# Performance work log

Hardware: AMD Instinct MI355X
Metric: run time of the kernel (lower is better)

The kernel has to match this reference:

```python
import jax, jax.numpy as jnp
import numpy as np
import math

NLAT, NLON, LMAX, MMAX = 128, 256, 50, 50
K = 3  # three_nn

# ---- precompute: Clenshaw-Curtis quadrature (torch_harmonics 'equiangular') ----
def _cc_nodes_weights(n):
    Nn = n - 1
    theta = np.pi * np.arange(n) / Nn
    v = np.zeros(n)
    for k in range(1, Nn // 2 + 1):
        b = 1.0 if 2 * k == Nn else 2.0
        v += b * np.cos(2 * k * theta) / (4 * k * k - 1)
    w = (2.0 / Nn) * (1.0 - v)
    w[0] *= 0.5
    w[-1] *= 0.5
    return np.cos(theta), w

# ---- precompute: orthonormal associated Legendre P_l^m(cos theta), csphase ----
def _legpoly(lmax, mmax, cost):
    sint = np.sqrt(np.clip(1.0 - cost ** 2, 0.0, None))
    p = np.zeros((mmax, lmax, cost.shape[0]))
    pmm = np.full(cost.shape[0], np.sqrt(1.0 / (4.0 * np.pi)))
    for m in range(mmax):
        if m > 0:
            pmm = -pmm * np.sqrt((2.0 * m + 1.0) / (2.0 * m)) * sint
        p[m, m] = pmm
        if m + 1 < lmax:
            p[m, m + 1] = np.sqrt(2.0 * m + 3.0) * cost * pmm
        for l in range(m + 2, lmax):
            a = np.sqrt((4.0 * l * l - 1.0) / (l * l - m * m))
            b = np.sqrt(((2.0 * l + 1.0) * (l - 1 + m) * (l - 1 - m)) / ((2.0 * l - 3.0) * (l * l - m * m)))
            p[m, l] = a * cost * p[m, l - 1] - b * p[m, l - 2]
    return p

_cost, _w = _cc_nodes_weights(NLAT)
_PCTW = jnp.asarray((_legpoly(LMAX, MMAX, _cost) * _w[None, None, :]).astype(np.float32))  # (mmax,lmax,nlat)

_gx, _gy = np.meshgrid(np.arange(NLAT), np.arange(-NLAT, NLAT), indexing='ij')
_GRID = jnp.asarray((np.stack([_gx.ravel(), _gy.ravel()], -1) / NLAT * np.pi).astype(np.float32))  # (M,2)

_RECTW = jnp.asarray(np.exp(-(LMAX - np.arange(1, LMAX + 1)) ** 2 / (2.0 * LMAX ** 2)).astype(np.float32))  # (lmax,)


def to_spherical(coords):
    # coords: (B,N,3) -> r:(B,N), sph:(B,N,2) = [arccos(x/r), azimuth in [0,2pi)]
    sq = coords ** 2
    pn = jnp.sqrt(jnp.flip(jnp.cumsum(jnp.flip(sq, -1), -1), -1))  # pn[...,i] = ||coords[...,i:]||
    r = pn[..., 0]
    phi = jnp.arccos(coords[..., :-2] / pn[..., :-2])
    a = jnp.arccos(coords[..., -2] / pn[..., -2])
    phi_final = a + (2.0 * math.pi - 2.0 * a) * (coords[..., -1] < 0)
    return r, jnp.concatenate([phi, phi_final[..., None]], axis=-1)


def interp_to_grid(coords):
    # spherical transform + 3-NN (squared dists) + distance-weighted interpolation onto the lat/lon grid
    r, sph = to_spherical(coords)
    sph = sph.at[..., 1].add(-math.pi)
    # brute-force pairwise squared distances grid(M,2) vs sph(B,N,2): (B,M,N)
    d2 = (jnp.sum(_GRID ** 2, -1)[None, :, None] + jnp.sum(sph ** 2, -1)[:, None, :]
          - 2.0 * jnp.einsum('md,bnd->bmn', _GRID, sph))
    _, idx = jax.lax.top_k(-jax.lax.stop_gradient(d2), K)  # (B,M,K), ascending distance
    sel = jax.vmap(lambda s, i: s[i])(sph, idx)            # (B,M,K,2)
    fsel = jax.vmap(lambda f, i: f[i])(r, idx)             # (B,M,K)
    dk = jnp.sum((_GRID[None, :, None, :] - sel) ** 2, -1)  # recompute selected sq-dists (differentiable)
    w = dk / jnp.sum(dk, -1, keepdims=True)                # weights = dist / sum(dist), as in source
    return jnp.sum(fsel * w, -1).reshape(-1, NLAT, NLON)


def sht_real(x):
    # RealSHT (equiangular, ortho): rfft(norm='forward')*2pi, then Legendre*quadrature einsum; real part only
    xf = jnp.fft.rfft(x, axis=-1)[..., :MMAX] * (2.0 * math.pi / NLON)
    return jnp.einsum('bkm,mlk->blm', jnp.real(xf).astype(jnp.float32), _PCTW)  # (B,lmax,mmax)


def setup_inputs() -> dict:
    key = jax.random.key(0)
    k1, k2 = jax.random.split(key)
    pred = jax.random.normal(k1, (2, 2048, 3), dtype=jnp.float32)
    target = jax.random.normal(k2, (2, 2048, 3), dtype=jnp.float32)
    return {"pred": pred, "target": target}


def reference(pred, target):
    pc = sht_real(interp_to_grid(pred))
    tc = sht_real(interp_to_grid(target))
    return jnp.mean(jnp.sum((pc - tc) ** 2 * _RECTW[None, :, None], axis=(1, 2)))
```

## Files before the change

### kernel.cpp

```cpp
#include <hip/hip_runtime.h>
#include <math.h>

#define PI_D 3.14159265358979323846
#define PIF  3.14159265358979323846f
#define NLAT 128
#define NLON 256
#define LMAX 50
#define MMAX 50
#define NPTS 2048
#define NBT 16
#define NBA 32
#define NBIN (NBT * NBA)
#define WBIN 0.19634954084936207f
#define INVW 5.092958178940651f
#define BIG 1e30f
#define KMASK 0xFFFFF800u

__device__ __forceinline__ void insert3(float kf, float& k0, float& k1, float& k2) {
    float n1 = __builtin_amdgcn_fmed3f(kf, k0, k1);
    float n2 = __builtin_amdgcn_fmed3f(kf, k1, k2);
    k0 = fminf(kf, k0);
    k1 = n1;
    k2 = n2;
}

__device__ __forceinline__ float mkkey(float gt, float gl, float2 tl, int idx) {
    float dt = gt - tl.x, dl = gl - tl.y;
    float d = fmaf(dt, dt, dl * dl);
    return __uint_as_float((__float_as_uint(d) & KMASK) | (unsigned)idx);
}

__global__ __launch_bounds__(256) void fused_main(
    const float* __restrict__ pred, const float* __restrict__ tgt,
    float* __restrict__ pctwT, float* __restrict__ fre, float* __restrict__ out) {

    __shared__ float2 s_btl[NPTS];
    __shared__ float  s_br[NPTS];
    __shared__ int    s_cnt[NBIN];
    __shared__ int    s_off[NBIN + 1];
    __shared__ float  ctab[NLON];
    __shared__ float  row[NLON];
    __shared__ float  part[256];

    int bid = blockIdx.x;
    int t = threadIdx.x;

    if (bid >= 512) {
        int k = bid - 512;
        int m = t;
        if (k == 0 && m == 0) out[0] = 0.0f;
        if (m >= MMAX) return;

        double thd = PI_D * (double)k / 127.0;
        float cost = (float)cos(thd);
        float sint = (float)sin(thd);

        float c2 = (float)cos(2.0 * thd);
        float two_c2 = 2.0f * c2;
        float cp = 1.0f, cc = c2, v = 0.0f;
        for (int tt = 1; tt <= 63; ++tt) {
            v += 2.0f * cc / (float)(4 * tt * tt - 1);
            float cn = two_c2 * cc - cp;
            cp = cc;
            cc = cn;
        }
        float w = (2.0f / 127.0f) * (1.0f - v);
        if (k == 0 || k == 127) w *= 0.5f;

        float pmm = sqrtf(1.0f / (4.0f * PIF));
        for (int i = 1; i <= m; ++i)
            pmm = -pmm * sqrtf((2.0f * (float)i + 1.0f) / (2.0f * (float)i)) * sint;

        float* o = pctwT + (size_t)k * MMAX + m;
        for (int l = 0; l < m; ++l) o[(size_t)l * NLAT * MMAX] = 0.0f;
        o[(size_t)m * NLAT * MMAX] = pmm * w;
        float plm2 = pmm, plm1 = 0.0f;
        if (m + 1 < LMAX) {
            plm1 = sqrtf(2.0f * (float)m + 3.0f) * cost * pmm;
            o[(size_t)(m + 1) * NLAT * MMAX] = plm1 * w;
        }
        for (int l = m + 2; l < LMAX; ++l) {
            float fl = (float)l;
            float denom = fl * fl - (float)(m * m);
            float a = sqrtf((4.0f * fl * fl - 1.0f) / denom);
            float b = sqrtf(((2.0f * fl + 1.0f) * (float)(l - 1 + m) * (float)(l - 1 - m)) /
                            ((2.0f * fl - 3.0f) * denom));
            float p = a * cost * plm1 - b * plm2;
            o[(size_t)l * NLAT * MMAX] = p * w;
            plm2 = plm1;
            plm1 = p;
        }
        return;
    }

    int f = bid >> 7;
    int lat = bid & 127;
    const float* src = ((f < 2) ? pred : tgt) + (size_t)(f & 1) * NPTS * 3;

    s_cnt[t] = 0;
    s_cnt[t + 256] = 0;
    ctab[t] = (float)cos(2.0 * PI_D * (double)t / (double)NLON);
    __syncthreads();

    float pth[8], paz[8], pr[8];
    int pbin[8];
#pragma unroll
    for (int i = 0; i < 8; ++i) {
        int n = t + 256 * i;
        float x = src[3 * n], y = src[3 * n + 1], z = src[3 * n + 2];
        float s1 = z * z;
        float s2 = s1 + y * y;
        float s3 = s2 + x * x;
        float r = sqrtf(s3);
        float rho = sqrtf(s2);
        float th = acosf(x / r);
        float a = acosf(y / rho);
        float az = (z < 0.0f) ? (a + (2.0f * PIF - 2.0f * a)) : a;
        az -= PIF;
        int bt = min(max((int)(th * INVW), 0), NBT - 1);
        int ba = min(max((int)((az + PIF) * INVW), 0), NBA - 1);
        int b = bt * NBA + ba;
        pth[i] = th; paz[i] = az; pr[i] = r; pbin[i] = b;
        atomicAdd(&s_cnt[b], 1);
    }
    __syncthreads();

    if (t == 0) s_off[NBIN] = NPTS;
    if (t < 64) {
        int base = t * 8;
        int loc[8];
        int run = 0;
#pragma unroll
        for (int i = 0; i < 8; ++i) { loc[i] = run; run += s_cnt[base + i]; }
        int x = run;
#pragma unroll
        for (int d = 1; d < 64; d <<= 1) {
            int y = __shfl_up(x, d);
            if (t >= d) x += y;
        }
        int ex = x - run;
#pragma unroll
        for (int i = 0; i < 8; ++i) s_off[base + i] = ex + loc[i];
    }
    __syncthreads();
    s_cnt[t] = s_off[t];
    s_cnt[t + 256] = s_off[t + 256];
    __syncthreads();
#pragma unroll
    for (int i = 0; i < 8; ++i) {
        int pos = atomicAdd(&s_cnt[pbin[i]], 1);
        s_btl[pos] = make_float2(pth[i], paz[i]);
        s_br[pos] = pr[i];
    }
    __syncthreads();

    int j = t;
    float gt = (float)((double)lat * PI_D / 128.0);
    float gl = (float)(((double)j - 128.0) * PI_D / 128.0);
    float glp = gl + PIF;
    int bt0 = lat >> 3;
    int ba0 = j >> 3;

    auto scan_seg = [&](int i, int i1, float& q0, float& q1, float& q2) {
        for (; i + 4 <= i1; i += 4) {
            float2 a0 = s_btl[i];
            float2 a1 = s_btl[i + 1];
            float2 a2 = s_btl[i + 2];
            float2 a3 = s_btl[i + 3];
            insert3(mkkey(gt, gl, a0, i), q0, q1, q2);
            insert3(mkkey(gt, gl, a1, i + 1), q0, q1, q2);
            insert3(mkkey(gt, gl, a2, i + 2), q0, q1, q2);
            insert3(mkkey(gt, gl, a3, i + 3), q0, q1, q2);
        }
        for (; i < i1; ++i)
            insert3(mkkey(gt, gl, s_btl[i], i), q0, q1, q2);
    };

    float k0 = BIG, k1 = BIG, k2 = BIG;
    {
        int rtl = max(bt0 - 1, 0), rth = min(bt0 + 1, NBT - 1);
        int bal = max(ba0 - 1, 0), bah = min(ba0 + 1, NBA - 1);
        for (int bt = rtl; bt <= rth; ++bt)
            scan_seg(s_off[bt * NBA + bal], s_off[bt * NBA + bah + 1], k0, k1, k2);
    }

    bool done;
    {
        float safe = BIG;
        if (bt0 - 1 > 0)       safe = fminf(safe, gt - (float)(bt0 - 1) * WBIN);
        if (bt0 + 1 < NBT - 1) safe = fminf(safe, (float)(bt0 + 2) * WBIN - gt);
        if (ba0 - 1 > 0)       safe = fminf(safe, glp - (float)(ba0 - 1) * WBIN);
        if (ba0 + 1 < NBA - 1) safe = fminf(safe, (float)(ba0 + 2) * WBIN - glp);
        done = (k2 <= safe * safe);
    }

    for (int R = 2; R <= 31; ++R) {
        if (__all(done)) break;
        if (!done) {
            int btl = bt0 - R, bth = bt0 + R;
            int lo = max(btl, 0), hi = min(bth, NBT - 1);
            int bal = max(ba0 - R, 0), bah = min(ba0 + R, NBA - 1);
            for (int bt = lo; bt <= hi; ++bt) {
                if (bt == btl || bt == bth) {
                    scan_seg(s_off[bt * NBA + bal], s_off[bt * NBA + bah + 1], k0, k1, k2);
                } else {
                    if (ba0 - R >= 0) {
                        int b = bt * NBA + ba0 - R;
                        scan_seg(s_off[b], s_off[b + 1], k0, k1, k2);
                    }
                    if (ba0 + R <= NBA - 1) {
                        int b = bt * NBA + ba0 + R;
                        scan_seg(s_off[b], s_off[b + 1], k0, k1, k2);
                    }
                }
            }
            float safe = BIG;
            if (bt0 - R > 0)       safe = fminf(safe, gt - (float)(bt0 - R) * WBIN);
            if (bt0 + R < NBT - 1) safe = fminf(safe, (float)(bt0 + R + 1) * WBIN - gt);
            if (ba0 - R > 0)       safe = fminf(safe, glp - (float)(ba0 - R) * WBIN);
            if (ba0 + R < NBA - 1) safe = fminf(safe, (float)(ba0 + R + 1) * WBIN - glp);
            if (k2 <= safe * safe) done = true;
        }
    }

    {
        int i0 = __float_as_uint(k0) & 0x7FF;
        int i1 = __float_as_uint(k1) & 0x7FF;
        int i2 = __float_as_uint(k2) & 0x7FF;
        float2 p0 = s_btl[i0];
        float2 p1 = s_btl[i1];
        float2 p2 = s_btl[i2];
        float dt0 = gt - p0.x, dl0 = gl - p0.y;
        float dt1 = gt - p1.x, dl1 = gl - p1.y;
        float dt2 = gt - p2.x, dl2 = gl - p2.y;
        float d0 = fmaf(dt0, dt0, dl0 * dl0);
        float d1 = fmaf(dt1, dt1, dl1 * dl1);
        float d2 = fmaf(dt2, dt2, dl2 * dl2);
        float s = d0 + d1 + d2;
        row[j] = (d0 * s_br[i0] + d1 * s_br[i1] + d2 * s_br[i2]) / s;
    }
    __syncthreads();

    {
        int q = t >> 6;
        int mm = t & 63;
        if (mm < MMAX) {
            int bs = q * 64;
            float a0 = 0.0f, a1 = 0.0f, a2 = 0.0f, a3 = 0.0f;
            int p = (bs * mm) & (NLON - 1);
            int st1 = mm;
            int st2 = (2 * mm) & (NLON - 1);
            int st3 = (3 * mm) & (NLON - 1);
            int st4 = (4 * mm) & (NLON - 1);
            for (int i = 0; i < 64; i += 4) {
                a0 += row[bs + i] * ctab[p];
                a1 += row[bs + i + 1] * ctab[(p + st1) & (NLON - 1)];
                a2 += row[bs + i + 2] * ctab[(p + st2) & (NLON - 1)];
                a3 += row[bs + i + 3] * ctab[(p + st3) & (NLON - 1)];
                p = (p + st4) & (NLON - 1);
            }
            part[q * 64 + mm] = (a0 + a1) + (a2 + a3);
        }
    }
    __syncthreads();
    if (t < MMAX) {
        float v = ((part[t] + part[64 + t]) + (part[128 + t] + part[192 + t])) *
                  (float)(2.0 * PI_D / (double)NLON);
        fre[(f * NLAT + lat) * MMAX + t] = v;
    }
}

__global__ __launch_bounds__(256) void contract_loss(const float* __restrict__ fre,
                                                     const float* __restrict__ pctwT,
                                                     float* __restrict__ out) {
    int b = blockIdx.x / LMAX;
    int l = blockIdx.x % LMAX;
    int mm = threadIdx.x & 63;
    int kq = threadIdx.x >> 6;
    __shared__ float sp[4][64], st_[4][64];
    float pc = 0.0f, tc = 0.0f;
    if (mm < MMAX) {
        const float* pw = pctwT + ((size_t)l * NLAT + kq * 32) * MMAX + mm;
        const float* fp = fre + ((size_t)b * NLAT + kq * 32) * MMAX + mm;
        const float* ft = fre + ((size_t)(2 + b) * NLAT + kq * 32) * MMAX + mm;
#pragma unroll 8
        for (int k = 0; k < 32; ++k) {
            float w = pw[k * MMAX];
            pc += fp[k * MMAX] * w;
            tc += ft[k * MMAX] * w;
        }
    }
    sp[kq][mm] = pc;
    st_[kq][mm] = tc;
    __syncthreads();
    if (threadIdx.x < 64) {
        int m2 = threadIdx.x;
        float pcs = (sp[0][m2] + sp[1][m2]) + (sp[2][m2] + sp[3][m2]);
        float tcs = (st_[0][m2] + st_[1][m2]) + (st_[2][m2] + st_[3][m2]);
        float diff = pcs - tcs;
        double dl_ = (double)(49 - l);
        float rw = (float)exp(-(dl_ * dl_) / 5000.0);
        float contrib = (m2 < MMAX) ? diff * diff * rw * 0.5f : 0.0f;
        for (int off = 32; off > 0; off >>= 1) contrib += __shfl_down(contrib, off);
        if (m2 == 0) atomicAdd(out, contrib);
    }
}

extern "C" void kernel_launch(void* const* d_in, const int* in_sizes, int n_in,
                              void* d_out, int out_size, void* d_ws, size_t ws_size,
                              hipStream_t stream) {
    const float* pred = (const float*)d_in[0];
    const float* tgt = (const float*)d_in[1];
    float* ws = (float*)d_ws;

    float* pctwT = ws;
    float* fre   = ws + 320000;
    float* out = (float*)d_out;

    fused_main<<<640, 256, 0, stream>>>(pred, tgt, pctwT, fre, out);
    contract_loss<<<2 * LMAX, 256, 0, stream>>>(fre, pctwT, out);
}
```

Measured before the change: 84.11 us.

## Merge main and contraction kernels into one cooperative launch with grid sync

Replaces the two-kernel sequence with a single cooperative kernel that runs the grid/Legendre stage, performs a grid-wide sync, then has the first 100 blocks do the Legendre contraction and loss reduction, reusing shared memory. This removes one kernel launch and the inter-kernel gap. In exchange it adds cooperative launch overhead and a grid barrier, and requires all 640 blocks to be co-resident. The cos table also switches from double cos to the fast __cosf intrinsic, trading accuracy for speed.

```diff
diff --git a/kernel.cpp b/kernel.cpp
--- a/kernel.cpp
+++ b/kernel.cpp
@@ -1,5 +1,8 @@
 #include <hip/hip_runtime.h>
+#include <hip/hip_cooperative_groups.h>
 #include <math.h>
+
+namespace cg = cooperative_groups;
 
 #define PI_D 3.14159265358979323846
 #define PIF  3.14159265358979323846f
@@ -30,7 +33,7 @@
     return __uint_as_float((__float_as_uint(d) & KMASK) | (unsigned)idx);
 }
 
-__global__ __launch_bounds__(256) void fused_main(
+__global__ __launch_bounds__(256) void mega_kernel(
     const float* __restrict__ pred, const float* __restrict__ tgt,
     float* __restrict__ pctwT, float* __restrict__ fre, float* __restrict__ out) {
 
@@ -42,6 +45,7 @@
     __shared__ float  row[NLON];
     __shared__ float  part[256];
 
+    cg::grid_group grid = cg::this_grid();
     int bid = blockIdx.x;
     int t = threadIdx.x;
 
@@ -49,260 +53,261 @@
         int k = bid - 512;
         int m = t;
         if (k == 0 && m == 0) out[0] = 0.0f;
-        if (m >= MMAX) return;
-
-        double thd = PI_D * (double)k / 127.0;
-        float cost = (float)cos(thd);
-        float sint = (float)sin(thd);
-
-        float c2 = (float)cos(2.0 * thd);
-        float two_c2 = 2.0f * c2;
-        float cp = 1.0f, cc = c2, v = 0.0f;
-        for (int tt = 1; tt <= 63; ++tt) {
-            v += 2.0f * cc / (float)(4 * tt * tt - 1);
-            float cn = two_c2 * cc - cp;
-            cp = cc;
-            cc = cn;
-        }
-        float w = (2.0f / 127.0f) * (1.0f - v);
-        if (k == 0 || k == 127) w *= 0.5f;
-
-        float pmm = sqrtf(1.0f / (4.0f * PIF));
-        for (int i = 1; i <= m; ++i)
-            pmm = -pmm * sqrtf((2.0f * (float)i + 1.0f) / (2.0f * (float)i)) * sint;
-
-        float* o = pctwT + (size_t)k * MMAX + m;
-        for (int l = 0; l < m; ++l) o[(size_t)l * NLAT * MMAX] = 0.0f;
-        o[(size_t)m * NLAT * MMAX] = pmm * w;
-        float plm2 = pmm, plm1 = 0.0f;
-        if (m + 1 < LMAX) {
-            plm1 = sqrtf(2.0f * (float)m + 3.0f) * cost * pmm;
-            o[(size_t)(m + 1) * NLAT * MMAX] = plm1 * w;
-        }
-        for (int l = m + 2; l < LMAX; ++l) {
-            float fl = (float)l;
-            float denom = fl * fl - (float)(m * m);
-            float a = sqrtf((4.0f * fl * fl - 1.0f) / denom);
-            float b = sqrtf(((2.0f * fl + 1.0f) * (float)(l - 1 + m) * (float)(l - 1 - m)) /
-                            ((2.0f * fl - 3.0f) * denom));
-            float p = a * cost * plm1 - b * plm2;
-            o[(size_t)l * NLAT * MMAX] = p * w;
-            plm2 = plm1;
-            plm1 = p;
-        }
-        return;
-    }
-
-    int f = bid >> 7;
-    int lat = bid & 127;
-    const float* src = ((f < 2) ? pred : tgt) + (size_t)(f & 1) * NPTS * 3;
-
-    s_cnt[t] = 0;
-    s_cnt[t + 256] = 0;
-    ctab[t] = (float)cos(2.0 * PI_D * (double)t / (double)NLON);
-    __syncthreads();
-
-    float pth[8], paz[8], pr[8];
-    int pbin[8];
-#pragma unroll
-    for (int i = 0; i < 8; ++i) {
-        int n = t + 256 * i;
-        float x = src[3 * n], y = src[3 * n + 1], z = src[3 * n + 2];
-        float s1 = z * z;
-        float s2 = s1 + y * y;
-        float s3 = s2 + x * x;
-        float r = sqrtf(s3);
-        float rho = sqrtf(s2);
-        float th = acosf(x / r);
-        float a = acosf(y / rho);
-        float az = (z < 0.0f) ? (a + (2.0f * PIF - 2.0f * a)) : a;
-        az -= PIF;
-        int bt = min(max((int)(th * INVW), 0), NBT - 1);
-        int ba = min(max((int)((az + PIF) * INVW), 0), NBA - 1);
-        int b = bt * NBA + ba;
-        pth[i] = th; paz[i] = az; pr[i] = r; pbin[i] = b;
-        atomicAdd(&s_cnt[b], 1);
-    }
-    __syncthreads();
-
-    if (t == 0) s_off[NBIN] = NPTS;
-    if (t < 64) {
-        int base = t * 8;
-        int loc[8];
-        int run = 0;
-#pragma unroll
-        for (int i = 0; i < 8; ++i) { loc[i] = run; run += s_cnt[base + i]; }
-        int x = run;
-#pragma unroll
-        for (int d = 1; d < 64; d <<= 1) {
-            int y = __shfl_up(x, d);
-            if (t >= d) x += y;
-        }
-        int ex = x - run;
-#pragma unroll
-        for (int i = 0; i < 8; ++i) s_off[base + i] = ex + loc[i];
-    }
-    __syncthreads();
-    s_cnt[t] = s_off[t];
-    s_cnt[t + 256] = s_off[t + 256];
-    __syncthreads();
-#pragma unroll
-    for (int i = 0; i < 8; ++i) {
-        int pos = atomicAdd(&s_cnt[pbin[i]], 1);
-        s_btl[pos] = make_float2(pth[i], paz[i]);
-        s_br[pos] = pr[i];
-    }
-    __syncthreads();
-
-    int j = t;
-    float gt = (float)((double)lat * PI_D / 128.0);
-    float gl = (float)(((double)j - 128.0) * PI_D / 128.0);
-    float glp = gl + PIF;
-    int bt0 = lat >> 3;
-    int ba0 = j >> 3;
-
-    auto scan_seg = [&](int i, int i1, float& q0, float& q1, float& q2) {
-        for (; i + 4 <= i1; i += 4) {
-            float2 a0 = s_btl[i];
-            float2 a1 = s_btl[i + 1];
-            float2 a2 = s_btl[i + 2];
-            float2 a3 = s_btl[i + 3];
-            insert3(mkkey(gt, gl, a0, i), q0, q1, q2);
-            insert3(mkkey(gt, gl, a1, i + 1), q0, q1, q2);
-            insert3(mkkey(gt, gl, a2, i + 2), q0, q1, q2);
-            insert3(mkkey(gt, gl, a3, i + 3), q0, q1, q2);
-        }
-        for (; i < i1; ++i)
-            insert3(mkkey(gt, gl, s_btl[i], i), q0, q1, q2);
-    };
-
-    float k0 = BIG, k1 = BIG, k2 = BIG;
-    {
-        int rtl = max(bt0 - 1, 0), rth = min(bt0 + 1, NBT - 1);
-        int bal = max(ba0 - 1, 0), bah = min(ba0 + 1, NBA - 1);
-        for (int bt = rtl; bt <= rth; ++bt)
-            scan_seg(s_off[bt * NBA + bal], s_off[bt * NBA + bah + 1], k0, k1, k2);
-    }
-
-    bool done;
-    {
-        float safe = BIG;
-        if (bt0 - 1 > 0)       safe = fminf(safe, gt - (float)(bt0 - 1) * WBIN);
-        if (bt0 + 1 < NBT - 1) safe = fminf(safe, (float)(bt0 + 2) * WBIN - gt);
-        if (ba0 - 1 > 0)       safe = fminf(safe, glp - (float)(ba0 - 1) * WBIN);
-        if (ba0 + 1 < NBA - 1) safe = fminf(safe, (float)(ba0 + 2) * WBIN - glp);
-        done = (k2 <= safe * safe);
-    }
-
-    for (int R = 2; R <= 31; ++R) {
-        if (__all(done)) break;
-        if (!done) {
-            int btl = bt0 - R, bth = bt0 + R;
-            int lo = max(btl, 0), hi = min(bth, NBT - 1);
-            int bal = max(ba0 - R, 0), bah = min(ba0 + R, NBA - 1);
-            for (int bt = lo; bt <= hi; ++bt) {
-                if (bt == btl || bt == bth) {
-                    scan_seg(s_off[bt * NBA + bal], s_off[bt * NBA + bah + 1], k0, k1, k2);
-                } else {
-                    if (ba0 - R >= 0) {
-                        int b = bt * NBA + ba0 - R;
-                        scan_seg(s_off[b], s_off[b + 1], k0, k1, k2);
-                    }
-                    if (ba0 + R <= NBA - 1) {
-                        int b = bt * NBA + ba0 + R;
-                        scan_seg(s_off[b], s_off[b + 1], k0, k1, k2);
+        if (m < MMAX) {
+            double thd = PI_D * (double)k / 127.0;
+            float cost = (float)cos(thd);
+            float sint = (float)sin(thd);
+
+            float c2 = (float)cos(2.0 * thd);
+            float two_c2 = 2.0f * c2;
+            float cp = 1.0f, cc = c2, v = 0.0f;
+            for (int tt = 1; tt <= 63; ++tt) {
+                v += 2.0f * cc / (float)(4 * tt * tt - 1);
+                float cn = two_c2 * cc - cp;
+                cp = cc;
+                cc = cn;
+            }
+            float w = (2.0f / 127.0f) * (1.0f - v);
+            if (k == 0 || k == 127) w *= 0.5f;
+
+            float pmm = sqrtf(1.0f / (4.0f * PIF));
+            for (int i = 1; i <= m; ++i)
+                pmm = -pmm * sqrtf((2.0f * (float)i + 1.0f) / (2.0f * (float)i)) * sint;
+
+            float* o = pctwT + (size_t)k * MMAX + m;
+            for (int l = 0; l < m; ++l) o[(size_t)l * NLAT * MMAX] = 0.0f;
+            o[(size_t)m * NLAT * MMAX] = pmm * w;
+            float plm2 = pmm, plm1 = 0.0f;
+            if (m + 1 < LMAX) {
+                plm1 = sqrtf(2.0f * (float)m + 3.0f) * cost * pmm;
+                o[(size_t)(m + 1) * NLAT * MMAX] = plm1 * w;
+            }
+            for (int l = m + 2; l < LMAX; ++l) {
+                float fl = (float)l;
+                float denom = fl * fl - (float)(m * m);
+                float a = sqrtf((4.0f * fl * fl - 1.0f) / denom);
+                float b = sqrtf(((2.0f * fl + 1.0f) * (float)(l - 1 + m) * (float)(l - 1 - m)) /
+                                ((2.0f * fl - 3.0f) * denom));
+                float p = a * cost * plm1 - b * plm2;
+                o[(size_t)l * NLAT * MMAX] = p * w;
+                plm2 = plm1;
+                plm1 = p;
+            }
+        }
+    } else {
+        int f = bid >> 7;
+        int lat = bid & 127;
+        const float* src = ((f < 2) ? pred : tgt) + (size_t)(f & 1) * NPTS * 3;
+
+        s_cnt[t] = 0;
+        s_cnt[t + 256] = 0;
+        ctab[t] = __cosf(2.0f * PIF * (float)t / (float)NLON);
+        __syncthreads();
+
+        float pth[8], paz[8], pr[8];
+        int pbin[8];
+#pragma unroll
+        for (int i = 0; i < 8; ++i) {
+            int n = t + 256 * i;
+            float x = src[3 * n], y = src[3 * n + 1], z = src[3 * n + 2];
+            float s1 = z * z;
+            float s2 = s1 + y * y;
+            float s3 = s2 + x * x;
+            float r = sqrtf(s3);
+            float rho = sqrtf(s2);
+            float th = acosf(x / r);
+            float a = acosf(y / rho);
+            float az = (z < 0.0f) ? (a + (2.0f * PIF - 2.0f * a)) : a;
+            az -= PIF;
+            int bt = min(max((int)(th * INVW), 0), NBT - 1);
+            int ba = min(max((int)((az + PIF) * INVW), 0), NBA - 1);
+            int b = bt * NBA + ba;
+            pth[i] = th; paz[i] = az; pr[i] = r; pbin[i] = b;
+            atomicAdd(&s_cnt[b], 1);
+        }
+        __syncthreads();
+
+        if (t == 0) s_off[NBIN] = NPTS;
+        if (t < 64) {
+            int base = t * 8;
+            int loc[8];
+            int run = 0;
+#pragma unroll
+            for (int i = 0; i < 8; ++i) { loc[i] = run; run += s_cnt[base + i]; }
+            int x = run;
+#pragma unroll
+            for (int d = 1; d < 64; d <<= 1) {
+                int y = __shfl_up(x, d);
+                if (t >= d) x += y;
+            }
+            int ex = x - run;
+#pragma unroll
+            for (int i = 0; i < 8; ++i) s_off[base + i] = ex + loc[i];
+        }
+        __syncthreads();
+        s_cnt[t] = s_off[t];
+        s_cnt[t + 256] = s_off[t + 256];
+        __syncthreads();
+#pragma unroll
+        for (int i = 0; i < 8; ++i) {
+            int pos = atomicAdd(&s_cnt[pbin[i]], 1);
+            s_btl[pos] = make_float2(pth[i], paz[i]);
+            s_br[pos] = pr[i];
+        }
+        __syncthreads();
+
+        int j = t;
+        float gt = (float)((double)lat * PI_D / 128.0);
+        float gl = (float)(((double)j - 128.0) * PI_D / 128.0);
+        float glp = gl + PIF;
+        int bt0 = lat >> 3;
+        int ba0 = j >> 3;
+
+        auto scan_seg = [&](int i, int i1, float& q0, float& q1, float& q2) {
+            for (; i + 4 <= i1; i += 4) {
+                float2 a0 = s_btl[i];
+                float2 a1 = s_btl[i + 1];
+                float2 a2 = s_btl[i + 2];
+                float2 a3 = s_btl[i + 3];
+                insert3(mkkey(gt, gl, a0, i), q0, q1, q2);
+                insert3(mkkey(gt, gl, a1, i + 1), q0, q1, q2);
+                insert3(mkkey(gt, gl, a2, i + 2), q0, q1, q2);
+                insert3(mkkey(gt, gl, a3, i + 3), q0, q1, q2);
+            }
+            for (; i < i1; ++i)
+                insert3(mkkey(gt, gl, s_btl[i], i), q0, q1, q2);
+        };
+
+        float k0 = BIG, k1 = BIG, k2 = BIG;
+        {
+            int rtl = max(bt0 - 1, 0), rth = min(bt0 + 1, NBT - 1);
+            int bal = max(ba0 - 1, 0), bah = min(ba0 + 1, NBA - 1);
+            for (int bt = rtl; bt <= rth; ++bt)
+                scan_seg(s_off[bt * NBA + bal], s_off[bt * NBA + bah + 1], k0, k1, k2);
+        }
+
+        bool done;
+        {
+            float safe = BIG;
+            if (bt0 - 1 > 0)       safe = fminf(safe, gt - (float)(bt0 - 1) * WBIN);
+            if (bt0 + 1 < NBT - 1) safe = fminf(safe, (float)(bt0 + 2) * WBIN - gt);
+            if (ba0 - 1 > 0)       safe = fminf(safe, glp - (float)(ba0 - 1) * WBIN);
+            if (ba0 + 1 < NBA - 1) safe = fminf(safe, (float)(ba0 + 2) * WBIN - glp);
+            done = (k2 <= safe * safe);
+        }
+
+        for (int R = 2; R <= 31; ++R) {
+            if (__all(done)) break;
+            if (!done) {
+                int btl = bt0 - R, bth = bt0 + R;
+                int lo = max(btl, 0), hi = min(bth, NBT - 1);
+                int bal = max(ba0 - R, 0), bah = min(ba0 + R, NBA - 1);
+                for (int bt = lo; bt <= hi; ++bt) {
+                    if (bt == btl || bt == bth) {
+                        scan_seg(s_off[bt * NBA + bal], s_off[bt * NBA + bah + 1], k0, k1, k2);
+                    } else {
+                        if (ba0 - R >= 0) {
+                            int b = bt * NBA + ba0 - R;
+                            scan_seg(s_off[b], s_off[b + 1], k0, k1, k2);
+                        }
+                        if (ba0 + R <= NBA - 1) {
+                            int b = bt * NBA + ba0 + R;
+                            scan_seg(s_off[b], s_off[b + 1], k0, k1, k2);
+                        }
                     }
                 }
-            }
-            float safe = BIG;
-            if (bt0 - R > 0)       safe = fminf(safe, gt - (float)(bt0 - R) * WBIN);
-            if (bt0 + R < NBT - 1) safe = fminf(safe, (float)(bt0 + R + 1) * WBIN - gt);
-            if (ba0 - R > 0)       safe = fminf(safe, glp - (float)(ba0 - R) * WBIN);
-            if (ba0 + R < NBA - 1) safe = fminf(safe, (float)(ba0 + R + 1) * WBIN - glp);
-            if (k2 <= safe * safe) done = true;
+                float safe = BIG;
+                if (bt0 - R > 0)       safe = fminf(safe, gt - (float)(bt0 - R) * WBIN);
+                if (bt0 + R < NBT - 1) safe = fminf(safe, (float)(bt0 + R + 1) * WBIN - gt);
+                if (ba0 - R > 0)       safe = fminf(safe, glp - (float)(ba0 - R) * WBIN);
+                if (ba0 + R < NBA - 1) safe = fminf(safe, (float)(ba0 + R + 1) * WBIN - glp);
+                if (k2 <= safe * safe) done = true;
+            }
+        }
+
+        {
+            int i0 = __float_as_uint(k0) & 0x7FF;
+            int i1 = __float_as_uint(k1) & 0x7FF;
+            int i2 = __float_as_uint(k2) & 0x7FF;
+            float2 p0 = s_btl[i0];
+            float2 p1 = s_btl[i1];
+            float2 p2 = s_btl[i2];
+            float dt0 = gt - p0.x, dl0 = gl - p0.y;
+            float dt1 = gt - p1.x, dl1 = gl - p1.y;
+            float dt2 = gt - p2.x, dl2 = gl - p2.y;
+            float d0 = fmaf(dt0, dt0, dl0 * dl0);
+            float d1 = fmaf(dt1, dt1, dl1 * dl1);
+            float d2 = fmaf(dt2, dt2, dl2 * dl2);
+            float s = d0 + d1 + d2;
+            row[j] = (d0 * s_br[i0] + d1 * s_br[i1] + d2 * s_br[i2]) / s;
+        }
+        __syncthreads();
+
+        {
+            int q = t >> 6;
+            int mm = t & 63;
+            if (mm < MMAX) {
+                int bs = q * 64;
+                float a0 = 0.0f, a1 = 0.0f, a2 = 0.0f, a3 = 0.0f;
+                int p = (bs * mm) & (NLON - 1);
+                int st1 = mm;
+                int st2 = (2 * mm) & (NLON - 1);
+                int st3 = (3 * mm) & (NLON - 1);
+                int st4 = (4 * mm) & (NLON - 1);
+                for (int i = 0; i < 64; i += 4) {
+                    a0 += row[bs + i] * ctab[p];
+                    a1 += row[bs + i + 1] * ctab[(p + st1) & (NLON - 1)];
+                    a2 += row[bs + i + 2] * ctab[(p + st2) & (NLON - 1)];
+                    a3 += row[bs + i + 3] * ctab[(p + st3) & (NLON - 1)];
+                    p = (p + st4) & (NLON - 1);
+                }
+                part[q * 64 + mm] = (a0 + a1) + (a2 + a3);
+            }
+        }
+        __syncthreads();
+        if (t < MMAX) {
+            float v = ((part[t] + part[64 + t]) + (part[128 + t] + part[192 + t])) *
+                      (float)(2.0 * PI_D / (double)NLON);
+            fre[(f * NLAT + lat) * MMAX + t] = v;
         }
     }
 
-    {
-        int i0 = __float_as_uint(k0) & 0x7FF;
-        int i1 = __float_as_uint(k1) & 0x7FF;
-        int i2 = __float_as_uint(k2) & 0x7FF;
-        float2 p0 = s_btl[i0];
-        float2 p1 = s_btl[i1];
-        float2 p2 = s_btl[i2];
-        float dt0 = gt - p0.x, dl0 = gl - p0.y;
-        float dt1 = gt - p1.x, dl1 = gl - p1.y;
-        float dt2 = gt - p2.x, dl2 = gl - p2.y;
-        float d0 = fmaf(dt0, dt0, dl0 * dl0);
-        float d1 = fmaf(dt1, dt1, dl1 * dl1);
-        float d2 = fmaf(dt2, dt2, dl2 * dl2);
-        float s = d0 + d1 + d2;
-        row[j] = (d0 * s_br[i0] + d1 * s_br[i1] + d2 * s_br[i2]) / s;
-    }
-    __syncthreads();
-
-    {
-        int q = t >> 6;
+    __threadfence();
+    grid.sync();
+
+    if (bid < 2 * LMAX) {
+        int b = bid / LMAX;
+        int l = bid % LMAX;
         int mm = t & 63;
+        int kq = t >> 6;
+        float* spp = (float*)s_btl;
+        float* stt = spp + 256;
+        float pc = 0.0f, tc = 0.0f;
         if (mm < MMAX) {
-            int bs = q * 64;
-            float a0 = 0.0f, a1 = 0.0f, a2 = 0.0f, a3 = 0.0f;
-            int p = (bs * mm) & (NLON - 1);
-            int st1 = mm;
-            int st2 = (2 * mm) & (NLON - 1);
-            int st3 = (3 * mm) & (NLON - 1);
-            int st4 = (4 * mm) & (NLON - 1);
-            for (int i = 0; i < 64; i += 4) {
-                a0 += row[bs + i] * ctab[p];
-                a1 += row[bs + i + 1] * ctab[(p + st1) & (NLON - 1)];
-                a2 += row[bs + i + 2] * ctab[(p + st2) & (NLON - 1)];
-                a3 += row[bs + i + 3] * ctab[(p + st3) & (NLON - 1)];
-                p = (p + st4) & (NLON - 1);
-            }
-            part[q * 64 + mm] = (a0 + a1) + (a2 + a3);
-        }
-    }
-    __syncthreads();
-    if (t < MMAX) {
-        float v = ((part[t] + part[64 + t]) + (part[128 + t] + part[192 + t])) *
-                  (float)(2.0 * PI_D / (double)NLON);
-        fre[(f * NLAT + lat) * MMAX + t] = v;
-    }
-}
-
-__global__ __launch_bounds__(256) void contract_loss(const float* __restrict__ fre,
-                                                     const float* __restrict__ pctwT,
-                                                     float* __restrict__ out) {
-    int b = blockIdx.x / LMAX;
-    int l = blockIdx.x % LMAX;
-    int mm = threadIdx.x & 63;
-    int kq = threadIdx.x >> 6;
-    __shared__ float sp[4][64], st_[4][64];
-    float pc = 0.0f, tc = 0.0f;
-    if (mm < MMAX) {
-        const float* pw = pctwT + ((size_t)l * NLAT + kq * 32) * MMAX + mm;
-        const float* fp = fre + ((size_t)b * NLAT + kq * 32) * MMAX + mm;
-        const float* ft = fre + ((size_t)(2 + b) * NLAT + kq * 32) * MMAX + mm;
+            const float* pw = pctwT + ((size_t)l * NLAT + kq * 32) * MMAX + mm;
+            const float* fp = fre + ((size_t)b * NLAT + kq * 32) * MMAX + mm;
+            const float* ft = fre + ((size_t)(2 + b) * NLAT + kq * 32) * MMAX + mm;
 #pragma unroll 8
-        for (int k = 0; k < 32; ++k) {
-            float w = pw[k * MMAX];
-            pc += fp[k * MMAX] * w;
-            tc += ft[k * MMAX] * w;
-        }
-    }
-    sp[kq][mm] = pc;
-    st_[kq][mm] = tc;
-    __syncthreads();
-    if (threadIdx.x < 64) {
-        int m2 = threadIdx.x;
-        float pcs = (sp[0][m2] + sp[1][m2]) + (sp[2][m2] + sp[3][m2]);
-        float tcs = (st_[0][m2] + st_[1][m2]) + (st_[2][m2] + st_[3][m2]);
-        float diff = pcs - tcs;
-        double dl_ = (double)(49 - l);
-        float rw = (float)exp(-(dl_ * dl_) / 5000.0);
-        float contrib = (m2 < MMAX) ? diff * diff * rw * 0.5f : 0.0f;
-        for (int off = 32; off > 0; off >>= 1) contrib += __shfl_down(contrib, off);
-        if (m2 == 0) atomicAdd(out, contrib);
+            for (int k = 0; k < 32; ++k) {
+                float w = pw[k * MMAX];
+                pc += fp[k * MMAX] * w;
+                tc += ft[k * MMAX] * w;
+            }
+        }
+        spp[kq * 64 + mm] = pc;
+        stt[kq * 64 + mm] = tc;
+        __syncthreads();
+        if (t < 64) {
+            int m2 = t;
+            float pcs = (spp[m2] + spp[64 + m2]) + (spp[128 + m2] + spp[192 + m2]);
+            float tcs = (stt[m2] + stt[64 + m2]) + (stt[128 + m2] + stt[192 + m2]);
+            float diff = pcs - tcs;
+            double dl_ = (double)(49 - l);
+            float rw = (float)exp(-(dl_ * dl_) / 5000.0);
+            float contrib = (m2 < MMAX) ? diff * diff * rw * 0.5f : 0.0f;
+            for (int off = 32; off > 0; off >>= 1) contrib += __shfl_down(contrib, off);
+            if (m2 == 0) atomicAdd(out, contrib);
+        }
     }
 }
 
@@ -317,6 +322,7 @@
     float* fre   = ws + 320000;
     float* out = (float*)d_out;
 
-    fused_main<<<640, 256, 0, stream>>>(pred, tgt, pctwT, fre, out);
-    contract_loss<<<2 * LMAX, 256, 0, stream>>>(fre, pctwT, out);
+    void* args[] = { (void*)&pred, (void*)&tgt, (void*)&pctwT, (void*)&fre, (void*)&out };
+    hipLaunchCooperativeKernel((const void*)mega_kernel, dim3(640), dim3(256),
+                               args, 0, stream);
 }
```

Result: slower. 226.3 us (+169.0%).

## Process two latitude rows per block and replace cosine table with recurrence

Applied to the files above, without the earlier changes.

Each main block now handles two latitude rows instead of one, halving the number of blocks that redo the per-block spherical conversion, binning and prefix-scan setup over all 2048 points. The shared cosine table is dropped, and the DFT cosines are generated per 16-element segment using a Chebyshev recurrence seeded with __cosf. This amortizes setup work and cuts LDS use, but the grid shrinks from 512 to 256 main blocks, which reduces parallelism on a large GPU. The recurrence and fast-math cosine also add small precision drift.

```diff
diff --git a/kernel.cpp b/kernel.cpp
--- a/kernel.cpp
+++ b/kernel.cpp
@@ -38,15 +38,14 @@
     __shared__ float  s_br[NPTS];
     __shared__ int    s_cnt[NBIN];
     __shared__ int    s_off[NBIN + 1];
-    __shared__ float  ctab[NLON];
     __shared__ float  row[NLON];
     __shared__ float  part[256];
 
     int bid = blockIdx.x;
     int t = threadIdx.x;
 
-    if (bid >= 512) {
-        int k = bid - 512;
+    if (bid >= 256) {
+        int k = bid - 256;
         int m = t;
         if (k == 0 && m == 0) out[0] = 0.0f;
         if (m >= MMAX) return;
@@ -93,13 +92,12 @@
         return;
     }
 
-    int f = bid >> 7;
-    int lat = bid & 127;
+    int f = bid >> 6;
+    int lat0 = (bid & 63) * 2;
     const float* src = ((f < 2) ? pred : tgt) + (size_t)(f & 1) * NPTS * 3;
 
     s_cnt[t] = 0;
     s_cnt[t + 256] = 0;
-    ctab[t] = (float)cos(2.0 * PI_D * (double)t / (double)NLON);
     __syncthreads();
 
     float pth[8], paz[8], pr[8];
@@ -155,118 +153,128 @@
     __syncthreads();
 
     int j = t;
-    float gt = (float)((double)lat * PI_D / 128.0);
     float gl = (float)(((double)j - 128.0) * PI_D / 128.0);
     float glp = gl + PIF;
-    int bt0 = lat >> 3;
     int ba0 = j >> 3;
 
-    auto scan_seg = [&](int i, int i1, float& q0, float& q1, float& q2) {
-        for (; i + 4 <= i1; i += 4) {
-            float2 a0 = s_btl[i];
-            float2 a1 = s_btl[i + 1];
-            float2 a2 = s_btl[i + 2];
-            float2 a3 = s_btl[i + 3];
-            insert3(mkkey(gt, gl, a0, i), q0, q1, q2);
-            insert3(mkkey(gt, gl, a1, i + 1), q0, q1, q2);
-            insert3(mkkey(gt, gl, a2, i + 2), q0, q1, q2);
-            insert3(mkkey(gt, gl, a3, i + 3), q0, q1, q2);
-        }
-        for (; i < i1; ++i)
-            insert3(mkkey(gt, gl, s_btl[i], i), q0, q1, q2);
-    };
-
-    float k0 = BIG, k1 = BIG, k2 = BIG;
-    {
-        int rtl = max(bt0 - 1, 0), rth = min(bt0 + 1, NBT - 1);
-        int bal = max(ba0 - 1, 0), bah = min(ba0 + 1, NBA - 1);
-        for (int bt = rtl; bt <= rth; ++bt)
-            scan_seg(s_off[bt * NBA + bal], s_off[bt * NBA + bah + 1], k0, k1, k2);
-    }
-
-    bool done;
-    {
-        float safe = BIG;
-        if (bt0 - 1 > 0)       safe = fminf(safe, gt - (float)(bt0 - 1) * WBIN);
-        if (bt0 + 1 < NBT - 1) safe = fminf(safe, (float)(bt0 + 2) * WBIN - gt);
-        if (ba0 - 1 > 0)       safe = fminf(safe, glp - (float)(ba0 - 1) * WBIN);
-        if (ba0 + 1 < NBA - 1) safe = fminf(safe, (float)(ba0 + 2) * WBIN - glp);
-        done = (k2 <= safe * safe);
-    }
-
-    for (int R = 2; R <= 31; ++R) {
-        if (__all(done)) break;
-        if (!done) {
-            int btl = bt0 - R, bth = bt0 + R;
-            int lo = max(btl, 0), hi = min(bth, NBT - 1);
-            int bal = max(ba0 - R, 0), bah = min(ba0 + R, NBA - 1);
-            for (int bt = lo; bt <= hi; ++bt) {
-                if (bt == btl || bt == bth) {
-                    scan_seg(s_off[bt * NBA + bal], s_off[bt * NBA + bah + 1], k0, k1, k2);
-                } else {
-                    if (ba0 - R >= 0) {
-                        int b = bt * NBA + ba0 - R;
-                        scan_seg(s_off[b], s_off[b + 1], k0, k1, k2);
-                    }
-                    if (ba0 + R <= NBA - 1) {
-                        int b = bt * NBA + ba0 + R;
-                        scan_seg(s_off[b], s_off[b + 1], k0, k1, k2);
+    for (int rr = 0; rr < 2; ++rr) {
+        int lat = lat0 + rr;
+        float gt = (float)((double)lat * PI_D / 128.0);
+        int bt0 = lat >> 3;
+
+        auto scan_seg = [&](int i, int i1, float& q0, float& q1, float& q2) {
+            for (; i + 4 <= i1; i += 4) {
+                float2 a0 = s_btl[i];
+                float2 a1 = s_btl[i + 1];
+                float2 a2 = s_btl[i + 2];
+                float2 a3 = s_btl[i + 3];
+                insert3(mkkey(gt, gl, a0, i), q0, q1, q2);
+                insert3(mkkey(gt, gl, a1, i + 1), q0, q1, q2);
+                insert3(mkkey(gt, gl, a2, i + 2), q0, q1, q2);
+                insert3(mkkey(gt, gl, a3, i + 3), q0, q1, q2);
+            }
+            for (; i < i1; ++i)
+                insert3(mkkey(gt, gl, s_btl[i], i), q0, q1, q2);
+        };
+
+        float k0 = BIG, k1 = BIG, k2 = BIG;
+        {
+            int rtl = max(bt0 - 1, 0), rth = min(bt0 + 1, NBT - 1);
+            int bal = max(ba0 - 1, 0), bah = min(ba0 + 1, NBA - 1);
+            for (int bt = rtl; bt <= rth; ++bt)
+                scan_seg(s_off[bt * NBA + bal], s_off[bt * NBA + bah + 1], k0, k1, k2);
+        }
+
+        bool done;
+        {
+            float safe = BIG;
+            if (bt0 - 1 > 0)       safe = fminf(safe, gt - (float)(bt0 - 1) * WBIN);
+            if (bt0 + 1 < NBT - 1) safe = fminf(safe, (float)(bt0 + 2) * WBIN - gt);
+            if (ba0 - 1 > 0)       safe = fminf(safe, glp - (float)(ba0 - 1) * WBIN);
+            if (ba0 + 1 < NBA - 1) safe = fminf(safe, (float)(ba0 + 2) * WBIN - glp);
+            done = (k2 <= safe * safe);
+        }
+
+        for (int R = 2; R <= 31; ++R) {
+            if (__all(done)) break;
+            if (!done) {
+                int btl = bt0 - R, bth = bt0 + R;
+                int lo = max(btl, 0), hi = min(bth, NBT - 1);
+                int bal = max(ba0 - R, 0), bah = min(ba0 + R, NBA - 1);
+                for (int bt = lo; bt <= hi; ++bt) {
+                    if (bt == btl || bt == bth) {
+                        scan_seg(s_off[bt * NBA + bal], s_off[bt * NBA + bah + 1], k0, k1, k2);
+                    } else {
+                        if (ba0 - R >= 0) {
+                            int b = bt * NBA + ba0 - R;
+                            scan_seg(s_off[b], s_off[b + 1], k0, k1, k2);
+                        }
+                        if (ba0 + R <= NBA - 1) {
+                            int b = bt * NBA + ba0 + R;
+                            scan_seg(s_off[b], s_off[b + 1], k0, k1, k2);
+                        }
                     }
                 }
+                float safe = BIG;
+                if (bt0 - R > 0)       safe = fminf(safe, gt - (float)(bt0 - R) * WBIN);
+                if (bt0 + R < NBT - 1) safe = fminf(safe, (float)(bt0 + R + 1) * WBIN - gt);
+                if (ba0 - R > 0)       safe = fminf(safe, glp - (float)(ba0 - R) * WBIN);
+                if (ba0 + R < NBA - 1) safe = fminf(safe, (float)(ba0 + R + 1) * WBIN - glp);
+                if (k2 <= safe * safe) done = true;
             }
-            float safe = BIG;
-            if (bt0 - R > 0)       safe = fminf(safe, gt - (float)(bt0 - R) * WBIN);
-            if (bt0 + R < NBT - 1) safe = fminf(safe, (float)(bt0 + R + 1) * WBIN - gt);
-            if (ba0 - R > 0)       safe = fminf(safe, glp - (float)(ba0 - R) * WBIN);
-            if (ba0 + R < NBA - 1) safe = fminf(safe, (float)(ba0 + R + 1) * WBIN - glp);
-            if (k2 <= safe * safe) done = true;
-        }
-    }
-
-    {
-        int i0 = __float_as_uint(k0) & 0x7FF;
-        int i1 = __float_as_uint(k1) & 0x7FF;
-        int i2 = __float_as_uint(k2) & 0x7FF;
-        float2 p0 = s_btl[i0];
-        float2 p1 = s_btl[i1];
-        float2 p2 = s_btl[i2];
-        float dt0 = gt - p0.x, dl0 = gl - p0.y;
-        float dt1 = gt - p1.x, dl1 = gl - p1.y;
-        float dt2 = gt - p2.x, dl2 = gl - p2.y;
-        float d0 = fmaf(dt0, dt0, dl0 * dl0);
-        float d1 = fmaf(dt1, dt1, dl1 * dl1);
-        float d2 = fmaf(dt2, dt2, dl2 * dl2);
-        float s = d0 + d1 + d2;
-        row[j] = (d0 * s_br[i0] + d1 * s_br[i1] + d2 * s_br[i2]) / s;
-    }
-    __syncthreads();
-
-    {
-        int q = t >> 6;
-        int mm = t & 63;
-        if (mm < MMAX) {
-            int bs = q * 64;
-            float a0 = 0.0f, a1 = 0.0f, a2 = 0.0f, a3 = 0.0f;
-            int p = (bs * mm) & (NLON - 1);
-            int st1 = mm;
-            int st2 = (2 * mm) & (NLON - 1);
-            int st3 = (3 * mm) & (NLON - 1);
-            int st4 = (4 * mm) & (NLON - 1);
-            for (int i = 0; i < 64; i += 4) {
-                a0 += row[bs + i] * ctab[p];
-                a1 += row[bs + i + 1] * ctab[(p + st1) & (NLON - 1)];
-                a2 += row[bs + i + 2] * ctab[(p + st2) & (NLON - 1)];
-                a3 += row[bs + i + 3] * ctab[(p + st3) & (NLON - 1)];
-                p = (p + st4) & (NLON - 1);
+        }
+
+        {
+            int i0 = __float_as_uint(k0) & 0x7FF;
+            int i1 = __float_as_uint(k1) & 0x7FF;
+            int i2 = __float_as_uint(k2) & 0x7FF;
+            float2 p0 = s_btl[i0];
+            float2 p1 = s_btl[i1];
+            float2 p2 = s_btl[i2];
+            float dt0 = gt - p0.x, dl0 = gl - p0.y;
+            float dt1 = gt - p1.x, dl1 = gl - p1.y;
+            float dt2 = gt - p2.x, dl2 = gl - p2.y;
+            float d0 = fmaf(dt0, dt0, dl0 * dl0);
+            float d1 = fmaf(dt1, dt1, dl1 * dl1);
+            float d2 = fmaf(dt2, dt2, dl2 * dl2);
+            float s = d0 + d1 + d2;
+            row[j] = (d0 * s_br[i0] + d1 * s_br[i1] + d2 * s_br[i2]) / s;
+        }
+        __syncthreads();
+
+        {
+            int q = t >> 6;
+            int mm = t & 63;
+            if (mm < MMAX) {
+                int bs = q * 64;
+                const float W0 = 2.0f * PIF / 256.0f;
+                float cphi2 = 2.0f * __cosf(W0 * (float)mm);
+                float acc = 0.0f;
+#pragma unroll
+                for (int seg = 0; seg < 4; ++seg) {
+                    int i0 = bs + seg * 16;
+                    float c0 = __cosf(W0 * (float)((i0 * mm) & 255));
+                    float c1 = __cosf(W0 * (float)(((i0 + 1) * mm) & 255));
+                    acc = fmaf(row[i0], c0, acc);
+                    acc = fmaf(row[i0 + 1], c1, acc);
+#pragma unroll
+                    for (int i = 2; i < 16; ++i) {
+                        float cn = fmaf(cphi2, c1, -c0);
+                        acc = fmaf(row[i0 + i], cn, acc);
+                        c0 = c1;
+                        c1 = cn;
+                    }
+                }
+                part[q * 64 + mm] = acc;
             }
-            part[q * 64 + mm] = (a0 + a1) + (a2 + a3);
-        }
-    }
-    __syncthreads();
-    if (t < MMAX) {
-        float v = ((part[t] + part[64 + t]) + (part[128 + t] + part[192 + t])) *
-                  (float)(2.0 * PI_D / (double)NLON);
-        fre[(f * NLAT + lat) * MMAX + t] = v;
+        }
+        __syncthreads();
+        if (t < MMAX) {
+            float v = ((part[t] + part[64 + t]) + (part[128 + t] + part[192 + t])) *
+                      (float)(2.0 * PI_D / (double)NLON);
+            fre[(f * NLAT + lat) * MMAX + t] = v;
+        }
+        __syncthreads();
     }
 }
 
@@ -317,6 +325,6 @@
     float* fre   = ws + 320000;
     float* out = (float*)d_out;
 
-    fused_main<<<640, 256, 0, stream>>>(pred, tgt, pctwT, fre, out);
+    fused_main<<<384, 256, 0, stream>>>(pred, tgt, pctwT, fre, out);
     contract_loss<<<2 * LMAX, 256, 0, stream>>>(fre, pctwT, out);
 }
```

Measured after the change: 82.11 us. -2.4%, faster.
